# Optimization experiments

Hardware: AMD Instinct MI355X
Metric: run time of the kernel (lower is better)

## Reference

```python
import jax, jax.numpy as jnp
import numpy as np

H = 4096          # hidden_size
M = 4096          # num tokens
BLK = 128         # fp8 quant group/block size
EPS = 1e-6
FP8_MAX = 448.0   # float8_e4m3fn max


def fp8_round(x):
    # round-trip through fp8 e4m3 to emulate FP8 storage
    return x.astype(jnp.float8_e4m3fn).astype(jnp.float32)


def rms_norm(x, w, eps=EPS):
    var = jnp.mean(x * x, axis=-1, keepdims=True)
    return x * jax.lax.rsqrt(var + eps) * w


def block_fp8_linear(x, w, wscale):
    # per-token group-128 activation quant + 128x128 block-scaled fp8 GEMM
    m, k = x.shape
    kb = k // BLK
    nb = w.shape[1] // BLK
    xr = x.reshape(m, kb, BLK)
    amax = jnp.max(jnp.abs(xr), axis=-1)                      # [m, kb]
    s = jnp.maximum(amax, 1e-12) / FP8_MAX                    # group scales
    q = fp8_round(xr / s[..., None])                          # fp8 values
    xdq = (q * s[..., None]).reshape(m, k)                    # dequant acts
    # dequantize weight blockwise: w already fp8-valued floats
    wdq = (w.reshape(kb, BLK, nb, BLK) * wscale[:, None, :, None]).reshape(k, nb * BLK)
    return xdq @ wdq


def setup_inputs() -> dict:
    key = jax.random.key(0)
    ks = jax.random.split(key, 8)
    x = jax.random.normal(ks[0], (M, H), dtype=jnp.float32)
    sb = H // BLK
    d = {"x": x}
    for i in range(3):
        w = fp8_round(jax.random.uniform(ks[1 + i], (H, H), dtype=jnp.float32)).T
        d[f"w{i}"] = w
        d[f"ws{i}"] = jax.random.uniform(ks[4 + i], (sb, sb), dtype=jnp.float32)
    for i in range(4):
        d[f"nw{i}"] = jnp.ones((H,), dtype=jnp.float32)
    return d


def reference(x, w0, ws0, w1, ws1, w2, ws2, nw0, nw1, nw2, nw3):
    x = jax.nn.relu(x)
    resid = x
    y = rms_norm(x, nw0)
    x2 = block_fp8_linear(y, w0, ws0)
    resid = x2 + resid
    y2 = rms_norm(resid, nw1)
    x3 = block_fp8_linear(y2, w1, ws1)
    resid = x3 + resid
    y3 = rms_norm(resid, nw2)
    x4 = block_fp8_linear(y3, w2, ws2)
    resid = x4 + resid
    y4 = rms_norm(resid, nw3)
    return y4
```

## Files before the change

kernel.cpp:

```cpp
#include <hip/hip_runtime.h>
#include <stdint.h>

#define H 4096

typedef float v4f __attribute__((ext_vector_type(4)));
typedef long long i64;
typedef long long v2l __attribute__((ext_vector_type(2)));

__device__ __forceinline__ void gload16(const uint8_t* g, uint8_t* l) {
  __builtin_amdgcn_global_load_lds(
      (const __attribute__((address_space(1))) uint8_t*)g,
      (__attribute__((address_space(3))) uint8_t*)l, 16, 0, 0);
}

__device__ __forceinline__ int permpos(int kg) {
  const int kb = kg >> 7, b = kg & 127;
  const int ks = b >> 5, q = (b >> 3) & 3, j = b & 7;
  return kb * 128 + q * 32 + ks * 8 + j;
}

__global__ __launch_bounds__(256) void conv_w_kernel(
    const float* __restrict__ w0, const float* __restrict__ w1,
    const float* __restrict__ w2, uint8_t* __restrict__ o0,
    uint8_t* __restrict__ o1, uint8_t* __restrict__ o2) {
  const float* w = (blockIdx.z == 0) ? w0 : (blockIdx.z == 1 ? w1 : w2);
  uint8_t* o = (blockIdx.z == 0) ? o0 : (blockIdx.z == 1 ? o1 : o2);
  __shared__ uint8_t t[64][136];
  const int tid = threadIdx.x;
  const int k0 = blockIdx.y * 128, n0 = blockIdx.x * 64;
  const int rr = tid >> 4, cc = (tid & 15) * 4;
#pragma unroll
  for (int j = 0; j < 8; ++j) {
    const int r = rr + j * 16;
    v4f f = *(const v4f*)(w + (size_t)(k0 + r) * H + n0 + cc);
    unsigned p = __builtin_amdgcn_cvt_pk_fp8_f32(f.x, f.y, 0, false);
    p = __builtin_amdgcn_cvt_pk_fp8_f32(f.z, f.w, p, true);
    t[cc + 0][r] = p & 0xff;
    t[cc + 1][r] = (p >> 8) & 0xff;
    t[cc + 2][r] = (p >> 16) & 0xff;
    t[cc + 3][r] = p >> 24;
  }
  __syncthreads();
#pragma unroll
  for (int i = 0; i < 2; ++i) {
    const int c = i * 256 + tid;
    const int n = c >> 3, o16 = c & 7, q = o16 >> 1, h = o16 & 1;
    long long lo = *(const long long*)&t[n][64 * h + q * 8];
    long long hi = *(const long long*)&t[n][64 * h + 32 + q * 8];
    v2l val;
    val.x = lo;
    val.y = hi;
    *(v2l*)(o + (size_t)(n0 + n) * H + k0 + o16 * 16) = val;
  }
}

__global__ __launch_bounds__(256) void quant_kernel(
    const float* in, const float* __restrict__ nw, uint8_t* __restrict__ q,
    float* __restrict__ sxT, const int relu) {
  const int row = blockIdx.x, tid = threadIdx.x;
  const v4f* rp = (const v4f*)(in + (size_t)row * H);
  v4f v[4];
  float ss = 0.f;
#pragma unroll
  for (int j = 0; j < 4; ++j) {
    v4f x = rp[j * 256 + tid];
    if (relu) {
      x.x = fmaxf(x.x, 0.f); x.y = fmaxf(x.y, 0.f);
      x.z = fmaxf(x.z, 0.f); x.w = fmaxf(x.w, 0.f);
    }
    v[j] = x;
    ss += x.x * x.x + x.y * x.y + x.z * x.z + x.w * x.w;
  }
#pragma unroll
  for (int o = 32; o > 0; o >>= 1) ss += __shfl_down(ss, o);
  __shared__ float red[4];
  if ((tid & 63) == 0) red[tid >> 6] = ss;
  __syncthreads();
  ss = red[0] + red[1] + red[2] + red[3];
  const float rinv = 1.f / sqrtf(ss * (1.f / H) + 1e-6f);
#pragma unroll
  for (int j = 0; j < 4; ++j) {
    v4f nv = ((const v4f*)nw)[j * 256 + tid];
    v4f y;
    y.x = v[j].x * rinv * nv.x;
    y.y = v[j].y * rinv * nv.y;
    y.z = v[j].z * rinv * nv.z;
    y.w = v[j].w * rinv * nv.w;
    float am = fmaxf(fmaxf(fabsf(y.x), fabsf(y.y)), fmaxf(fabsf(y.z), fabsf(y.w)));
#pragma unroll
    for (int o = 16; o > 0; o >>= 1) am = fmaxf(am, __shfl_xor(am, o, 32));
    const float s = fmaxf(am, 1e-12f) / 448.f;
    unsigned p = __builtin_amdgcn_cvt_pk_fp8_f32(y.x / s, y.y / s, 0, false);
    p = __builtin_amdgcn_cvt_pk_fp8_f32(y.z / s, y.w / s, p, true);
    const int col = (j * 256 + tid) * 4;
    *(unsigned*)(q + (size_t)row * H + permpos(col)) = p;
    if ((tid & 31) == 0)
      sxT[(size_t)(j * 8 + (tid >> 5)) * 4096 + row] = s;
  }
}

__global__ __launch_bounds__(256) void norm_kernel(float* io,
                                                   const float* __restrict__ nw) {
  const int row = blockIdx.x, tid = threadIdx.x;
  v4f* rp = (v4f*)(io + (size_t)row * H);
  v4f v[4];
  float ss = 0.f;
#pragma unroll
  for (int j = 0; j < 4; ++j) {
    v4f x = rp[j * 256 + tid];
    v[j] = x;
    ss += x.x * x.x + x.y * x.y + x.z * x.z + x.w * x.w;
  }
#pragma unroll
  for (int o = 32; o > 0; o >>= 1) ss += __shfl_down(ss, o);
  __shared__ float red[4];
  if ((tid & 63) == 0) red[tid >> 6] = ss;
  __syncthreads();
  ss = red[0] + red[1] + red[2] + red[3];
  const float rinv = 1.f / sqrtf(ss * (1.f / H) + 1e-6f);
#pragma unroll
  for (int j = 0; j < 4; ++j) {
    v4f nv = ((const v4f*)nw)[j * 256 + tid];
    v4f y;
    y.x = v[j].x * rinv * nv.x;
    y.y = v[j].y * rinv * nv.y;
    y.z = v[j].z * rinv * nv.z;
    y.w = v[j].w * rinv * nv.w;
    rp[j * 256 + tid] = y;
  }
}

__global__ __launch_bounds__(256, 4) void gemm_kernel(
    const uint8_t* __restrict__ qa,
    const float* __restrict__ sxT,
    const uint8_t* __restrict__ wt,
    const float* __restrict__ ws,
    const float* resid, float* outp, const int relu) {
  __shared__ __attribute__((aligned(16))) uint8_t sA[16384];
  __shared__ __attribute__((aligned(16))) uint8_t sB[16384];
  __shared__ __attribute__((aligned(16))) float scb[128];
  __shared__ float ws_s[32];

  const int tid = threadIdx.x;
  const int n0 = blockIdx.x * 128, m0 = blockIdx.y * 128;
  if (tid < 32) ws_s[tid] = ws[tid * 32 + blockIdx.x];

  const int wv = tid >> 6, lane = tid & 63;
  const int quad = lane >> 4, l16 = lane & 15;
  const int wm = wv >> 1, wn = wv & 1;

  const int swc = (tid & 7) ^ ((tid >> 3) & 7);
  const uint8_t* gA = qa + (size_t)(m0 + (tid >> 3)) * H + swc * 16;
  const uint8_t* gB = wt + (size_t)(n0 + (tid >> 3)) * H + swc * 16;
  const uint8_t* gS = (const uint8_t*)sxT + (size_t)m0 * 4 + lane * 16;
  uint8_t* lA = sA + wv * 1024;
  uint8_t* lB = sB + wv * 1024;

  int offp[2];
#pragma unroll
  for (int ksp = 0; ksp < 2; ++ksp)
    offp[ksp] = (((quad * 2 + ksp) ^ (l16 & 7)) << 4);
  const int arow = (wm * 64 + l16) * 128;
  const int brow = (wn * 64 + l16) * 128;
  const int scoff = wm * 64 + quad * 4;

  const v4f zf = {0.f, 0.f, 0.f, 0.f};
  v4f acc[4][4];
#pragma unroll
  for (int i = 0; i < 4; ++i)
#pragma unroll
    for (int j = 0; j < 4; ++j) acc[i][j] = zf;

  for (int kb = 0; kb < 32; ++kb) {
#pragma unroll
    for (int i = 0; i < 4; ++i) {
      gload16(gA + (size_t)i * (32 * H), lA + i * 4096);
      gload16(gB + (size_t)i * (32 * H), lB + i * 4096);
    }
    if (wv == 0 && lane < 32) gload16(gS + (size_t)kb * 16384, (uint8_t*)scb);
    gA += 128;
    gB += 128;
    __syncthreads();

    const float wsk = ws_s[kb];
    v2l bf[4][2];
#pragma unroll
    for (int tc = 0; tc < 4; ++tc)
#pragma unroll
      for (int ksp = 0; ksp < 2; ++ksp)
        bf[tc][ksp] = *(const v2l*)(sB + brow + tc * 2048 + offp[ksp]);

#pragma unroll
    for (int tr = 0; tr < 4; ++tr) {
      const v2l a0 = *(const v2l*)(sA + arow + tr * 2048 + offp[0]);
      const v2l a1 = *(const v2l*)(sA + arow + tr * 2048 + offp[1]);
      const v4f s4 = *(const v4f*)(scb + scoff + tr * 16) * wsk;
#pragma unroll
      for (int tc = 0; tc < 4; ++tc) {
        v4f p = __builtin_amdgcn_mfma_f32_16x16x32_fp8_fp8(a0.x, bf[tc][0].x, zf, 0, 0, 0);
        p = __builtin_amdgcn_mfma_f32_16x16x32_fp8_fp8(a0.y, bf[tc][0].y, p, 0, 0, 0);
        p = __builtin_amdgcn_mfma_f32_16x16x32_fp8_fp8(a1.x, bf[tc][1].x, p, 0, 0, 0);
        p = __builtin_amdgcn_mfma_f32_16x16x32_fp8_fp8(a1.y, bf[tc][1].y, p, 0, 0, 0);
        acc[tr][tc] += p * s4;
      }
    }
    __syncthreads();
  }

  const int mB = m0 + wm * 64 + quad * 4;
  const int nB = n0 + wn * 64 + l16;
#pragma unroll
  for (int tr = 0; tr < 4; ++tr) {
#pragma unroll
    for (int r = 0; r < 4; ++r) {
      const size_t rowOff = (size_t)(mB + tr * 16 + r) * H;
#pragma unroll
      for (int tc = 0; tc < 4; ++tc) {
        const size_t idx = rowOff + nB + tc * 16;
        float rv = resid[idx];
        if (relu) rv = fmaxf(rv, 0.f);
        outp[idx] = acc[tr][tc][r] + rv;
      }
    }
  }
}

extern "C" void kernel_launch(void* const* d_in, const int* in_sizes, int n_in,
                              void* d_out, int out_size, void* d_ws, size_t ws_size,
                              hipStream_t stream) {
  const float* x   = (const float*)d_in[0];
  const float* w0  = (const float*)d_in[1];
  const float* ws0 = (const float*)d_in[2];
  const float* w1  = (const float*)d_in[3];
  const float* ws1 = (const float*)d_in[4];
  const float* w2  = (const float*)d_in[5];
  const float* ws2 = (const float*)d_in[6];
  const float* nw0 = (const float*)d_in[7];
  const float* nw1 = (const float*)d_in[8];
  const float* nw2 = (const float*)d_in[9];
  const float* nw3 = (const float*)d_in[10];
  float* R = (float*)d_out;

  uint8_t* base = (uint8_t*)d_ws;
  uint8_t* wq0 = base;
  uint8_t* wq1 = base + ((size_t)16 << 20);
  uint8_t* wq2 = base + ((size_t)32 << 20);
  uint8_t* qa  = base + ((size_t)48 << 20);
  float* sa    = (float*)(base + ((size_t)64 << 20));

  conv_w_kernel<<<dim3(64, 32, 3), 256, 0, stream>>>(w0, w1, w2, wq0, wq1, wq2);

  quant_kernel<<<4096, 256, 0, stream>>>(x, nw0, qa, sa, 1);
  gemm_kernel<<<dim3(32, 32), 256, 0, stream>>>(qa, sa, wq0, ws0, x, R, 1);

  quant_kernel<<<4096, 256, 0, stream>>>(R, nw1, qa, sa, 0);
  gemm_kernel<<<dim3(32, 32), 256, 0, stream>>>(qa, sa, wq1, ws1, R, R, 0);

  quant_kernel<<<4096, 256, 0, stream>>>(R, nw2, qa, sa, 0);
  gemm_kernel<<<dim3(32, 32), 256, 0, stream>>>(qa, sa, wq2, ws2, R, R, 0);

  norm_kernel<<<4096, 256, 0, stream>>>(R, nw3);
}
```

Measured before the change: 686.0 us.

## Fuse all stages into one persistent cooperative kernel with grid syncs

Refactors each kernel body into a grid-stride device stage and runs weight conversion, quantization, three GEMMs and the final norm inside one cooperative persistent kernel separated by grid.sync(). The aim is to remove the launch gaps and tail effects between eight separate launches. The trade-off is that the grid is capped at what fits resident (up to 1024 blocks), so the GEMM and row stages run as persistent loops. Grid-wide barriers also add their own cost. The original multi-launch path is kept as a fallback if the cooperative launch fails.

```diff
diff --git a/kernel.cpp b/kernel.cpp
--- a/kernel.cpp
+++ b/kernel.cpp
@@ -1,11 +1,13 @@
 #include <hip/hip_runtime.h>
+#include <hip/hip_cooperative_groups.h>
 #include <stdint.h>
 
 #define H 4096
 
 typedef float v4f __attribute__((ext_vector_type(4)));
-typedef long long i64;
 typedef long long v2l __attribute__((ext_vector_type(2)));
+
+namespace cg = cooperative_groups;
 
 __device__ __forceinline__ void gload16(const uint8_t* g, uint8_t* l) {
   __builtin_amdgcn_global_load_lds(
@@ -19,215 +21,287 @@
   return kb * 128 + q * 32 + ks * 8 + j;
 }
 
+
+__device__ void conv_stage(const float* __restrict__ w0,
+                           const float* __restrict__ w1,
+                           const float* __restrict__ w2, uint8_t* o0,
+                           uint8_t* o1, uint8_t* o2, uint8_t* smem, int bid,
+                           int nb) {
+  uint8_t(*t)[136] = reinterpret_cast<uint8_t(*)[136]>(smem);
+  const int tid = threadIdx.x;
+  const int rr = tid >> 4, cc = (tid & 15) * 4;
+  for (int g = bid; g < 6144; g += nb) {
+    const int z = g >> 11, rem = g & 2047;
+    const int k0 = (rem >> 6) * 128, n0 = (rem & 63) * 64;
+    const float* w = (z == 0) ? w0 : (z == 1 ? w1 : w2);
+    uint8_t* o = (z == 0) ? o0 : (z == 1 ? o1 : o2);
+#pragma unroll
+    for (int j = 0; j < 8; ++j) {
+      const int r = rr + j * 16;
+      v4f f = *(const v4f*)(w + (size_t)(k0 + r) * H + n0 + cc);
+      unsigned p = __builtin_amdgcn_cvt_pk_fp8_f32(f.x, f.y, 0, false);
+      p = __builtin_amdgcn_cvt_pk_fp8_f32(f.z, f.w, p, true);
+      t[cc + 0][r] = p & 0xff;
+      t[cc + 1][r] = (p >> 8) & 0xff;
+      t[cc + 2][r] = (p >> 16) & 0xff;
+      t[cc + 3][r] = p >> 24;
+    }
+    __syncthreads();
+#pragma unroll
+    for (int i = 0; i < 2; ++i) {
+      const int c = i * 256 + tid;
+      const int n = c >> 3, o16 = c & 7, q = o16 >> 1, h = o16 & 1;
+      long long lo = *(const long long*)&t[n][64 * h + q * 8];
+      long long hi = *(const long long*)&t[n][64 * h + 32 + q * 8];
+      v2l val;
+      val.x = lo;
+      val.y = hi;
+      *(v2l*)(o + (size_t)(n0 + n) * H + k0 + o16 * 16) = val;
+    }
+    __syncthreads();
+  }
+}
+
+__device__ void quant_stage(const float* in, const float* __restrict__ nw,
+                            uint8_t* __restrict__ q, float* __restrict__ sxT,
+                            const int relu, uint8_t* smem, int bid, int nb) {
+  float* red = reinterpret_cast<float*>(smem);
+  const int tid = threadIdx.x;
+  for (int row = bid; row < 4096; row += nb) {
+    const v4f* rp = (const v4f*)(in + (size_t)row * H);
+    v4f v[4];
+    float ss = 0.f;
+#pragma unroll
+    for (int j = 0; j < 4; ++j) {
+      v4f x = rp[j * 256 + tid];
+      if (relu) {
+        x.x = fmaxf(x.x, 0.f); x.y = fmaxf(x.y, 0.f);
+        x.z = fmaxf(x.z, 0.f); x.w = fmaxf(x.w, 0.f);
+      }
+      v[j] = x;
+      ss += x.x * x.x + x.y * x.y + x.z * x.z + x.w * x.w;
+    }
+#pragma unroll
+    for (int o = 32; o > 0; o >>= 1) ss += __shfl_down(ss, o);
+    if ((tid & 63) == 0) red[tid >> 6] = ss;
+    __syncthreads();
+    ss = red[0] + red[1] + red[2] + red[3];
+    const float rinv = 1.f / sqrtf(ss * (1.f / H) + 1e-6f);
+#pragma unroll
+    for (int j = 0; j < 4; ++j) {
+      v4f nv = ((const v4f*)nw)[j * 256 + tid];
+      v4f y;
+      y.x = v[j].x * rinv * nv.x;
+      y.y = v[j].y * rinv * nv.y;
+      y.z = v[j].z * rinv * nv.z;
+      y.w = v[j].w * rinv * nv.w;
+      float am =
+          fmaxf(fmaxf(fabsf(y.x), fabsf(y.y)), fmaxf(fabsf(y.z), fabsf(y.w)));
+#pragma unroll
+      for (int o = 16; o > 0; o >>= 1) am = fmaxf(am, __shfl_xor(am, o, 32));
+      const float s = fmaxf(am, 1e-12f) / 448.f;
+      unsigned p = __builtin_amdgcn_cvt_pk_fp8_f32(y.x / s, y.y / s, 0, false);
+      p = __builtin_amdgcn_cvt_pk_fp8_f32(y.z / s, y.w / s, p, true);
+      const int col = (j * 256 + tid) * 4;
+      *(unsigned*)(q + (size_t)row * H + permpos(col)) = p;
+      if ((tid & 31) == 0)
+        sxT[(size_t)(j * 8 + (tid >> 5)) * 4096 + row] = s;
+    }
+    __syncthreads();
+  }
+}
+
+__device__ void norm_stage(float* io, const float* __restrict__ nw,
+                           uint8_t* smem, int bid, int nb) {
+  float* red = reinterpret_cast<float*>(smem);
+  const int tid = threadIdx.x;
+  for (int row = bid; row < 4096; row += nb) {
+    v4f* rp = (v4f*)(io + (size_t)row * H);
+    v4f v[4];
+    float ss = 0.f;
+#pragma unroll
+    for (int j = 0; j < 4; ++j) {
+      v4f x = rp[j * 256 + tid];
+      v[j] = x;
+      ss += x.x * x.x + x.y * x.y + x.z * x.z + x.w * x.w;
+    }
+#pragma unroll
+    for (int o = 32; o > 0; o >>= 1) ss += __shfl_down(ss, o);
+    if ((tid & 63) == 0) red[tid >> 6] = ss;
+    __syncthreads();
+    ss = red[0] + red[1] + red[2] + red[3];
+    const float rinv = 1.f / sqrtf(ss * (1.f / H) + 1e-6f);
+#pragma unroll
+    for (int j = 0; j < 4; ++j) {
+      v4f nv = ((const v4f*)nw)[j * 256 + tid];
+      v4f y;
+      y.x = v[j].x * rinv * nv.x;
+      y.y = v[j].y * rinv * nv.y;
+      y.z = v[j].z * rinv * nv.z;
+      y.w = v[j].w * rinv * nv.w;
+      rp[j * 256 + tid] = y;
+    }
+    __syncthreads();
+  }
+}
+
+__device__ void gemm_stage(const uint8_t* __restrict__ qa,
+                           const float* __restrict__ sxT,
+                           const uint8_t* __restrict__ wt,
+                           const float* __restrict__ ws, const float* resid,
+                           float* outp, const int relu, uint8_t* smem, int bid,
+                           int nb) {
+  uint8_t* sA = smem;
+  uint8_t* sB = smem + 16384;
+  float* scb = reinterpret_cast<float*>(smem + 32768);
+  float* ws_s = reinterpret_cast<float*>(smem + 33280);
+  const int tid = threadIdx.x;
+  const int wv = tid >> 6, lane = tid & 63;
+  const int quad = lane >> 4, l16 = lane & 15;
+  const int wm = wv >> 1, wn = wv & 1;
+  const int swc = (tid & 7) ^ ((tid >> 3) & 7);
+
+  for (int b = bid; b < 1024; b += nb) {
+    const int n0 = (b & 31) * 128, m0 = (b >> 5) * 128;
+    if (tid < 32) ws_s[tid] = ws[tid * 32 + (b & 31)];
+
+    const uint8_t* gA = qa + (size_t)(m0 + (tid >> 3)) * H + swc * 16;
+    const uint8_t* gB = wt + (size_t)(n0 + (tid >> 3)) * H + swc * 16;
+    const uint8_t* gS = (const uint8_t*)sxT + (size_t)m0 * 4 + lane * 16;
+    uint8_t* lA = sA + wv * 1024;
+    uint8_t* lB = sB + wv * 1024;
+
+    int offp[2];
+#pragma unroll
+    for (int ksp = 0; ksp < 2; ++ksp)
+      offp[ksp] = (((quad * 2 + ksp) ^ (l16 & 7)) << 4);
+    const int arow = (wm * 64 + l16) * 128;
+    const int brow = (wn * 64 + l16) * 128;
+    const int scoff = wm * 64 + quad * 4;
+
+    const v4f zf = {0.f, 0.f, 0.f, 0.f};
+    v4f acc[4][4];
+#pragma unroll
+    for (int i = 0; i < 4; ++i)
+#pragma unroll
+      for (int j = 0; j < 4; ++j) acc[i][j] = zf;
+
+    for (int kb = 0; kb < 32; ++kb) {
+#pragma unroll
+      for (int i = 0; i < 4; ++i) {
+        gload16(gA + (size_t)i * (32 * H), lA + i * 4096);
+        gload16(gB + (size_t)i * (32 * H), lB + i * 4096);
+      }
+      if (wv == 0 && lane < 32) gload16(gS + (size_t)kb * 16384, (uint8_t*)scb);
+      gA += 128;
+      gB += 128;
+      __syncthreads();
+
+      const float wsk = ws_s[kb];
+      v2l bf[4][2];
+#pragma unroll
+      for (int tc = 0; tc < 4; ++tc)
+#pragma unroll
+        for (int ksp = 0; ksp < 2; ++ksp)
+          bf[tc][ksp] = *(const v2l*)(sB + brow + tc * 2048 + offp[ksp]);
+
+#pragma unroll
+      for (int tr = 0; tr < 4; ++tr) {
+        const v2l a0 = *(const v2l*)(sA + arow + tr * 2048 + offp[0]);
+        const v2l a1 = *(const v2l*)(sA + arow + tr * 2048 + offp[1]);
+        const v4f s4 = *(const v4f*)(scb + scoff + tr * 16) * wsk;
+#pragma unroll
+        for (int tc = 0; tc < 4; ++tc) {
+          v4f p = __builtin_amdgcn_mfma_f32_16x16x32_fp8_fp8(a0.x, bf[tc][0].x, zf, 0, 0, 0);
+          p = __builtin_amdgcn_mfma_f32_16x16x32_fp8_fp8(a0.y, bf[tc][0].y, p, 0, 0, 0);
+          p = __builtin_amdgcn_mfma_f32_16x16x32_fp8_fp8(a1.x, bf[tc][1].x, p, 0, 0, 0);
+          p = __builtin_amdgcn_mfma_f32_16x16x32_fp8_fp8(a1.y, bf[tc][1].y, p, 0, 0, 0);
+          acc[tr][tc] += p * s4;
+        }
+      }
+      __syncthreads();
+    }
+
+    const int mB = m0 + wm * 64 + quad * 4;
+    const int nB = n0 + wn * 64 + l16;
+#pragma unroll
+    for (int tr = 0; tr < 4; ++tr) {
+#pragma unroll
+      for (int r = 0; r < 4; ++r) {
+        const size_t rowOff = (size_t)(mB + tr * 16 + r) * H;
+#pragma unroll
+        for (int tc = 0; tc < 4; ++tc) {
+          const size_t idx = rowOff + nB + tc * 16;
+          float rv = resid[idx];
+          if (relu) rv = fmaxf(rv, 0.f);
+          outp[idx] = acc[tr][tc][r] + rv;
+        }
+      }
+    }
+  }
+}
+
+__global__ __launch_bounds__(256, 4) void mega_kernel(
+    const float* x, const float* w0, const float* ws0, const float* w1,
+    const float* ws1, const float* w2, const float* ws2, const float* nw0,
+    const float* nw1, const float* nw2, const float* nw3, float* R,
+    uint8_t* wq0, uint8_t* wq1, uint8_t* wq2, uint8_t* qa, float* sa) {
+  __shared__ __attribute__((aligned(16))) uint8_t smem[33792];
+  cg::grid_group grid = cg::this_grid();
+  const int bid = blockIdx.x, nb = gridDim.x;
+
+  conv_stage(w0, w1, w2, wq0, wq1, wq2, smem, bid, nb);
+  quant_stage(x, nw0, qa, sa, 1, smem, bid, nb);
+  grid.sync();
+  gemm_stage(qa, sa, wq0, ws0, x, R, 1, smem, bid, nb);
+  grid.sync();
+  quant_stage(R, nw1, qa, sa, 0, smem, bid, nb);
+  grid.sync();
+  gemm_stage(qa, sa, wq1, ws1, R, R, 0, smem, bid, nb);
+  grid.sync();
+  quant_stage(R, nw2, qa, sa, 0, smem, bid, nb);
+  grid.sync();
+  gemm_stage(qa, sa, wq2, ws2, R, R, 0, smem, bid, nb);
+  grid.sync();
+  norm_stage(R, nw3, smem, bid, nb);
+}
+
 __global__ __launch_bounds__(256) void conv_w_kernel(
     const float* __restrict__ w0, const float* __restrict__ w1,
     const float* __restrict__ w2, uint8_t* __restrict__ o0,
     uint8_t* __restrict__ o1, uint8_t* __restrict__ o2) {
-  const float* w = (blockIdx.z == 0) ? w0 : (blockIdx.z == 1 ? w1 : w2);
-  uint8_t* o = (blockIdx.z == 0) ? o0 : (blockIdx.z == 1 ? o1 : o2);
-  __shared__ uint8_t t[64][136];
-  const int tid = threadIdx.x;
-  const int k0 = blockIdx.y * 128, n0 = blockIdx.x * 64;
-  const int rr = tid >> 4, cc = (tid & 15) * 4;
-#pragma unroll
-  for (int j = 0; j < 8; ++j) {
-    const int r = rr + j * 16;
-    v4f f = *(const v4f*)(w + (size_t)(k0 + r) * H + n0 + cc);
-    unsigned p = __builtin_amdgcn_cvt_pk_fp8_f32(f.x, f.y, 0, false);
-    p = __builtin_amdgcn_cvt_pk_fp8_f32(f.z, f.w, p, true);
-    t[cc + 0][r] = p & 0xff;
-    t[cc + 1][r] = (p >> 8) & 0xff;
-    t[cc + 2][r] = (p >> 16) & 0xff;
-    t[cc + 3][r] = p >> 24;
-  }
-  __syncthreads();
-#pragma unroll
-  for (int i = 0; i < 2; ++i) {
-    const int c = i * 256 + tid;
-    const int n = c >> 3, o16 = c & 7, q = o16 >> 1, h = o16 & 1;
-    long long lo = *(const long long*)&t[n][64 * h + q * 8];
-    long long hi = *(const long long*)&t[n][64 * h + 32 + q * 8];
-    v2l val;
-    val.x = lo;
-    val.y = hi;
-    *(v2l*)(o + (size_t)(n0 + n) * H + k0 + o16 * 16) = val;
-  }
-}
-
-__global__ __launch_bounds__(256) void quant_kernel(
-    const float* in, const float* __restrict__ nw, uint8_t* __restrict__ q,
-    float* __restrict__ sxT, const int relu) {
-  const int row = blockIdx.x, tid = threadIdx.x;
-  const v4f* rp = (const v4f*)(in + (size_t)row * H);
-  v4f v[4];
-  float ss = 0.f;
-#pragma unroll
-  for (int j = 0; j < 4; ++j) {
-    v4f x = rp[j * 256 + tid];
-    if (relu) {
-      x.x = fmaxf(x.x, 0.f); x.y = fmaxf(x.y, 0.f);
-      x.z = fmaxf(x.z, 0.f); x.w = fmaxf(x.w, 0.f);
-    }
-    v[j] = x;
-    ss += x.x * x.x + x.y * x.y + x.z * x.z + x.w * x.w;
-  }
-#pragma unroll
-  for (int o = 32; o > 0; o >>= 1) ss += __shfl_down(ss, o);
-  __shared__ float red[4];
-  if ((tid & 63) == 0) red[tid >> 6] = ss;
-  __syncthreads();
-  ss = red[0] + red[1] + red[2] + red[3];
-  const float rinv = 1.f / sqrtf(ss * (1.f / H) + 1e-6f);
-#pragma unroll
-  for (int j = 0; j < 4; ++j) {
-    v4f nv = ((const v4f*)nw)[j * 256 + tid];
-    v4f y;
-    y.x = v[j].x * rinv * nv.x;
-    y.y = v[j].y * rinv * nv.y;
-    y.z = v[j].z * rinv * nv.z;
-    y.w = v[j].w * rinv * nv.w;
-    float am = fmaxf(fmaxf(fabsf(y.x), fabsf(y.y)), fmaxf(fabsf(y.z), fabsf(y.w)));
-#pragma unroll
-    for (int o = 16; o > 0; o >>= 1) am = fmaxf(am, __shfl_xor(am, o, 32));
-    const float s = fmaxf(am, 1e-12f) / 448.f;
-    unsigned p = __builtin_amdgcn_cvt_pk_fp8_f32(y.x / s, y.y / s, 0, false);
-    p = __builtin_amdgcn_cvt_pk_fp8_f32(y.z / s, y.w / s, p, true);
-    const int col = (j * 256 + tid) * 4;
-    *(unsigned*)(q + (size_t)row * H + permpos(col)) = p;
-    if ((tid & 31) == 0)
-      sxT[(size_t)(j * 8 + (tid >> 5)) * 4096 + row] = s;
-  }
+  __shared__ __attribute__((aligned(16))) uint8_t smem[8704];
+  const int g = (blockIdx.z << 11) | (blockIdx.y << 6) | blockIdx.x;
+  conv_stage(w0, w1, w2, o0, o1, o2, smem, g, 6144);
+}
+
+__global__ __launch_bounds__(256) void quant_kernel(const float* in,
+                                                    const float* __restrict__ nw,
+                                                    uint8_t* __restrict__ q,
+                                                    float* __restrict__ sxT,
+                                                    const int relu) {
+  __shared__ __attribute__((aligned(16))) uint8_t smem[16];
+  quant_stage(in, nw, q, sxT, relu, smem, blockIdx.x, 4096);
 }
 
 __global__ __launch_bounds__(256) void norm_kernel(float* io,
                                                    const float* __restrict__ nw) {
-  const int row = blockIdx.x, tid = threadIdx.x;
-  v4f* rp = (v4f*)(io + (size_t)row * H);
-  v4f v[4];
-  float ss = 0.f;
-#pragma unroll
-  for (int j = 0; j < 4; ++j) {
-    v4f x = rp[j * 256 + tid];
-    v[j] = x;
-    ss += x.x * x.x + x.y * x.y + x.z * x.z + x.w * x.w;
-  }
-#pragma unroll
-  for (int o = 32; o > 0; o >>= 1) ss += __shfl_down(ss, o);
-  __shared__ float red[4];
-  if ((tid & 63) == 0) red[tid >> 6] = ss;
-  __syncthreads();
-  ss = red[0] + red[1] + red[2] + red[3];
-  const float rinv = 1.f / sqrtf(ss * (1.f / H) + 1e-6f);
-#pragma unroll
-  for (int j = 0; j < 4; ++j) {
-    v4f nv = ((const v4f*)nw)[j * 256 + tid];
-    v4f y;
-    y.x = v[j].x * rinv * nv.x;
-    y.y = v[j].y * rinv * nv.y;
-    y.z = v[j].z * rinv * nv.z;
-    y.w = v[j].w * rinv * nv.w;
-    rp[j * 256 + tid] = y;
-  }
+  __shared__ __attribute__((aligned(16))) uint8_t smem[16];
+  norm_stage(io, nw, smem, blockIdx.x, 4096);
 }
 
 __global__ __launch_bounds__(256, 4) void gemm_kernel(
-    const uint8_t* __restrict__ qa,
-    const float* __restrict__ sxT,
-    const uint8_t* __restrict__ wt,
-    const float* __restrict__ ws,
+    const uint8_t* __restrict__ qa, const float* __restrict__ sxT,
+    const uint8_t* __restrict__ wt, const float* __restrict__ ws,
     const float* resid, float* outp, const int relu) {
-  __shared__ __attribute__((aligned(16))) uint8_t sA[16384];
-  __shared__ __attribute__((aligned(16))) uint8_t sB[16384];
-  __shared__ __attribute__((aligned(16))) float scb[128];
-  __shared__ float ws_s[32];
-
-  const int tid = threadIdx.x;
-  const int n0 = blockIdx.x * 128, m0 = blockIdx.y * 128;
-  if (tid < 32) ws_s[tid] = ws[tid * 32 + blockIdx.x];
-
-  const int wv = tid >> 6, lane = tid & 63;
-  const int quad = lane >> 4, l16 = lane & 15;
-  const int wm = wv >> 1, wn = wv & 1;
-
-  const int swc = (tid & 7) ^ ((tid >> 3) & 7);
-  const uint8_t* gA = qa + (size_t)(m0 + (tid >> 3)) * H + swc * 16;
-  const uint8_t* gB = wt + (size_t)(n0 + (tid >> 3)) * H + swc * 16;
-  const uint8_t* gS = (const uint8_t*)sxT + (size_t)m0 * 4 + lane * 16;
-  uint8_t* lA = sA + wv * 1024;
-  uint8_t* lB = sB + wv * 1024;
-
-  int offp[2];
-#pragma unroll
-  for (int ksp = 0; ksp < 2; ++ksp)
-    offp[ksp] = (((quad * 2 + ksp) ^ (l16 & 7)) << 4);
-  const int arow = (wm * 64 + l16) * 128;
-  const int brow = (wn * 64 + l16) * 128;
-  const int scoff = wm * 64 + quad * 4;
-
-  const v4f zf = {0.f, 0.f, 0.f, 0.f};
-  v4f acc[4][4];
-#pragma unroll
-  for (int i = 0; i < 4; ++i)
-#pragma unroll
-    for (int j = 0; j < 4; ++j) acc[i][j] = zf;
-
-  for (int kb = 0; kb < 32; ++kb) {
-#pragma unroll
-    for (int i = 0; i < 4; ++i) {
-      gload16(gA + (size_t)i * (32 * H), lA + i * 4096);
-      gload16(gB + (size_t)i * (32 * H), lB + i * 4096);
-    }
-    if (wv == 0 && lane < 32) gload16(gS + (size_t)kb * 16384, (uint8_t*)scb);
-    gA += 128;
-    gB += 128;
-    __syncthreads();
-
-    const float wsk = ws_s[kb];
-    v2l bf[4][2];
-#pragma unroll
-    for (int tc = 0; tc < 4; ++tc)
-#pragma unroll
-      for (int ksp = 0; ksp < 2; ++ksp)
-        bf[tc][ksp] = *(const v2l*)(sB + brow + tc * 2048 + offp[ksp]);
-
-#pragma unroll
-    for (int tr = 0; tr < 4; ++tr) {
-      const v2l a0 = *(const v2l*)(sA + arow + tr * 2048 + offp[0]);
-      const v2l a1 = *(const v2l*)(sA + arow + tr * 2048 + offp[1]);
-      const v4f s4 = *(const v4f*)(scb + scoff + tr * 16) * wsk;
-#pragma unroll
-      for (int tc = 0; tc < 4; ++tc) {
-        v4f p = __builtin_amdgcn_mfma_f32_16x16x32_fp8_fp8(a0.x, bf[tc][0].x, zf, 0, 0, 0);
-        p = __builtin_amdgcn_mfma_f32_16x16x32_fp8_fp8(a0.y, bf[tc][0].y, p, 0, 0, 0);
-        p = __builtin_amdgcn_mfma_f32_16x16x32_fp8_fp8(a1.x, bf[tc][1].x, p, 0, 0, 0);
-        p = __builtin_amdgcn_mfma_f32_16x16x32_fp8_fp8(a1.y, bf[tc][1].y, p, 0, 0, 0);
-        acc[tr][tc] += p * s4;
-      }
-    }
-    __syncthreads();
-  }
-
-  const int mB = m0 + wm * 64 + quad * 4;
-  const int nB = n0 + wn * 64 + l16;
-#pragma unroll
-  for (int tr = 0; tr < 4; ++tr) {
-#pragma unroll
-    for (int r = 0; r < 4; ++r) {
-      const size_t rowOff = (size_t)(mB + tr * 16 + r) * H;
-#pragma unroll
-      for (int tc = 0; tc < 4; ++tc) {
-        const size_t idx = rowOff + nB + tc * 16;
-        float rv = resid[idx];
-        if (relu) rv = fmaxf(rv, 0.f);
-        outp[idx] = acc[tr][tc][r] + rv;
-      }
-    }
-  }
+  __shared__ __attribute__((aligned(16))) uint8_t smem[33792];
+  gemm_stage(qa, sxT, wt, ws, resid, outp, relu, smem,
+             blockIdx.y * 32 + blockIdx.x, 1024);
 }
 
 extern "C" void kernel_launch(void* const* d_in, const int* in_sizes, int n_in,
-                              void* d_out, int out_size, void* d_ws, size_t ws_size,
-                              hipStream_t stream) {
+                              void* d_out, int out_size, void* d_ws,
+                              size_t ws_size, hipStream_t stream) {
   const float* x   = (const float*)d_in[0];
   const float* w0  = (const float*)d_in[1];
   const float* ws0 = (const float*)d_in[2];
@@ -248,16 +322,36 @@
   uint8_t* qa  = base + ((size_t)48 << 20);
   float* sa    = (float*)(base + ((size_t)64 << 20));
 
-  conv_w_kernel<<<dim3(64, 32, 3), 256, 0, stream>>>(w0, w1, w2, wq0, wq1, wq2);
-
-  quant_kernel<<<4096, 256, 0, stream>>>(x, nw0, qa, sa, 1);
-  gemm_kernel<<<dim3(32, 32), 256, 0, stream>>>(qa, sa, wq0, ws0, x, R, 1);
-
-  quant_kernel<<<4096, 256, 0, stream>>>(R, nw1, qa, sa, 0);
-  gemm_kernel<<<dim3(32, 32), 256, 0, stream>>>(qa, sa, wq1, ws1, R, R, 0);
-
-  quant_kernel<<<4096, 256, 0, stream>>>(R, nw2, qa, sa, 0);
-  gemm_kernel<<<dim3(32, 32), 256, 0, stream>>>(qa, sa, wq2, ws2, R, R, 0);
-
-  norm_kernel<<<4096, 256, 0, stream>>>(R, nw3);
-}
+  static int grid_blocks = -1;
+  if (grid_blocks < 0) {
+    int per_cu = 0;
+    if (hipOccupancyMaxActiveBlocksPerMultiprocessor(
+            &per_cu, (const void*)mega_kernel, 256, 0) != hipSuccess ||
+        per_cu < 1)
+      per_cu = 0;
+    long long mb = (long long)per_cu * 256;
+    grid_blocks = (int)(mb > 1024 ? 1024 : mb);
+  }
+
+  bool ok = false;
+  if (grid_blocks >= 256) {
+    void* args[] = {(void*)&x,   (void*)&w0,  (void*)&ws0, (void*)&w1,
+                    (void*)&ws1, (void*)&w2,  (void*)&ws2, (void*)&nw0,
+                    (void*)&nw1, (void*)&nw2, (void*)&nw3, (void*)&R,
+                    (void*)&wq0, (void*)&wq1, (void*)&wq2, (void*)&qa,
+                    (void*)&sa};
+    ok = hipLaunchCooperativeKernel((const void*)mega_kernel,
+                                    dim3(grid_blocks), dim3(256), args, 0,
+                                    stream) == hipSuccess;
+  }
+  if (!ok) {
+    conv_w_kernel<<<dim3(64, 32, 3), 256, 0, stream>>>(w0, w1, w2, wq0, wq1, wq2);
+    quant_kernel<<<4096, 256, 0, stream>>>(x, nw0, qa, sa, 1);
+    gemm_kernel<<<dim3(32, 32), 256, 0, stream>>>(qa, sa, wq0, ws0, x, R, 1);
+    quant_kernel<<<4096, 256, 0, stream>>>(R, nw1, qa, sa, 0);
+    gemm_kernel<<<dim3(32, 32), 256, 0, stream>>>(qa, sa, wq1, ws1, R, R, 0);
+    quant_kernel<<<4096, 256, 0, stream>>>(R, nw2, qa, sa, 0);
+    gemm_kernel<<<dim3(32, 32), 256, 0, stream>>>(qa, sa, wq2, ws2, R, R, 0);
+    norm_kernel<<<4096, 256, 0, stream>>>(R, nw3);
+  }
+}
```

Result: slower. 1.671 ms (+143.5%).

## Fuse RMSNorm/quant into GEMM tail via per-row-block atomic counters

Applied to the files above, without the earlier changes.

Weight fp8 conversion and the first activation quantisation are merged into one prep kernel. Each GEMM now ends with an atomic counter per 128-row block. The last 16 tiles of a row block wait until all 32 column tiles are done, then run the next layer's RMSNorm+quant, or the final norm, for 8 rows each. This removes four standalone launches and the gaps between them, but adds spin-waiting and relies on all blocks being co-resident to avoid deadlock.

```diff
diff --git a/kernel.cpp b/kernel.cpp
--- a/kernel.cpp
+++ b/kernel.cpp
@@ -4,7 +4,6 @@
 #define H 4096
 
 typedef float v4f __attribute__((ext_vector_type(4)));
-typedef long long i64;
 typedef long long v2l __attribute__((ext_vector_type(2)));
 
 __device__ __forceinline__ void gload16(const uint8_t* g, uint8_t* l) {
@@ -19,15 +18,11 @@
   return kb * 128 + q * 32 + ks * 8 + j;
 }
 
-__global__ __launch_bounds__(256) void conv_w_kernel(
-    const float* __restrict__ w0, const float* __restrict__ w1,
-    const float* __restrict__ w2, uint8_t* __restrict__ o0,
-    uint8_t* __restrict__ o1, uint8_t* __restrict__ o2) {
-  const float* w = (blockIdx.z == 0) ? w0 : (blockIdx.z == 1 ? w1 : w2);
-  uint8_t* o = (blockIdx.z == 0) ? o0 : (blockIdx.z == 1 ? o1 : o2);
-  __shared__ uint8_t t[64][136];
+__device__ __forceinline__ void conv_tile(const float* __restrict__ w,
+                                          uint8_t* __restrict__ o, int k0,
+                                          int n0, uint8_t* smem) {
+  uint8_t(*t)[136] = reinterpret_cast<uint8_t(*)[136]>(smem);
   const int tid = threadIdx.x;
-  const int k0 = blockIdx.y * 128, n0 = blockIdx.x * 64;
   const int rr = tid >> 4, cc = (tid & 15) * 4;
 #pragma unroll
   for (int j = 0; j < 8; ++j) {
@@ -54,10 +49,11 @@
   }
 }
 
-__global__ __launch_bounds__(256) void quant_kernel(
-    const float* in, const float* __restrict__ nw, uint8_t* __restrict__ q,
-    float* __restrict__ sxT, const int relu) {
-  const int row = blockIdx.x, tid = threadIdx.x;
+__device__ __forceinline__ void quant_row(const float* in,
+                                          const float* __restrict__ nw,
+                                          uint8_t* q, float* sxT, int row,
+                                          int relu, float* red) {
+  const int tid = threadIdx.x;
   const v4f* rp = (const v4f*)(in + (size_t)row * H);
   v4f v[4];
   float ss = 0.f;
@@ -73,7 +69,6 @@
   }
 #pragma unroll
   for (int o = 32; o > 0; o >>= 1) ss += __shfl_down(ss, o);
-  __shared__ float red[4];
   if ((tid & 63) == 0) red[tid >> 6] = ss;
   __syncthreads();
   ss = red[0] + red[1] + red[2] + red[3];
@@ -86,7 +81,8 @@
     y.y = v[j].y * rinv * nv.y;
     y.z = v[j].z * rinv * nv.z;
     y.w = v[j].w * rinv * nv.w;
-    float am = fmaxf(fmaxf(fabsf(y.x), fabsf(y.y)), fmaxf(fabsf(y.z), fabsf(y.w)));
+    float am =
+        fmaxf(fmaxf(fabsf(y.x), fabsf(y.y)), fmaxf(fabsf(y.z), fabsf(y.w)));
 #pragma unroll
     for (int o = 16; o > 0; o >>= 1) am = fmaxf(am, __shfl_xor(am, o, 32));
     const float s = fmaxf(am, 1e-12f) / 448.f;
@@ -99,9 +95,9 @@
   }
 }
 
-__global__ __launch_bounds__(256) void norm_kernel(float* io,
-                                                   const float* __restrict__ nw) {
-  const int row = blockIdx.x, tid = threadIdx.x;
+__device__ __forceinline__ void norm_row(float* io, const float* __restrict__ nw,
+                                         int row, float* red) {
+  const int tid = threadIdx.x;
   v4f* rp = (v4f*)(io + (size_t)row * H);
   v4f v[4];
   float ss = 0.f;
@@ -113,7 +109,6 @@
   }
 #pragma unroll
   for (int o = 32; o > 0; o >>= 1) ss += __shfl_down(ss, o);
-  __shared__ float red[4];
   if ((tid & 63) == 0) red[tid >> 6] = ss;
   __syncthreads();
   ss = red[0] + red[1] + red[2] + red[3];
@@ -130,16 +125,40 @@
   }
 }
 
-__global__ __launch_bounds__(256, 4) void gemm_kernel(
-    const uint8_t* __restrict__ qa,
-    const float* __restrict__ sxT,
+__global__ __launch_bounds__(256) void prep_kernel(
+    const float* __restrict__ w0, const float* __restrict__ w1,
+    const float* __restrict__ w2, uint8_t* __restrict__ o0,
+    uint8_t* __restrict__ o1, uint8_t* __restrict__ o2, const float* x,
+    const float* __restrict__ nw0, uint8_t* qa, float* sa, int* sync0) {
+  __shared__ __attribute__((aligned(16))) uint8_t smem[8704];
+  const int bid = blockIdx.x;
+  if (bid == 0) {
+    for (int i = threadIdx.x; i < 3072; i += 256) sync0[i] = 0;
+  }
+  if (bid < 6144) {
+    const int z = bid >> 11, rem = bid & 2047;
+    const float* w = (z == 0) ? w0 : (z == 1 ? w1 : w2);
+    uint8_t* o = (z == 0) ? o0 : (z == 1 ? o1 : o2);
+    conv_tile(w, o, (rem >> 6) * 128, (rem & 63) * 64, smem);
+  } else {
+    quant_row(x, nw0, qa, sa, bid - 6144, 1, (float*)smem);
+  }
+}
+
+__global__ __launch_bounds__(256, 4) void gemm_fused_kernel(
+    const uint8_t* qa,
+    const float* sxT,
     const uint8_t* __restrict__ wt,
     const float* __restrict__ ws,
-    const float* resid, float* outp, const int relu) {
-  __shared__ __attribute__((aligned(16))) uint8_t sA[16384];
-  __shared__ __attribute__((aligned(16))) uint8_t sB[16384];
-  __shared__ __attribute__((aligned(16))) float scb[128];
-  __shared__ float ws_s[32];
+    const float* resid, float* outp, const int relu,
+    int* cnt,
+    const int tailmode,
+    uint8_t* qa2, float* sa2, const float* __restrict__ nwt) {
+  __shared__ __attribute__((aligned(16))) uint8_t smem[33792];
+  uint8_t* sA = smem;
+  uint8_t* sB = smem + 16384;
+  float* scb = reinterpret_cast<float*>(smem + 32768);
+  float* ws_s = reinterpret_cast<float*>(smem + 33280);
 
   const int tid = threadIdx.x;
   const int n0 = blockIdx.x * 128, m0 = blockIdx.y * 128;
@@ -223,11 +242,38 @@
       }
     }
   }
+
+  __threadfence();
+  __shared__ int rank_s;
+  if (tid == 0) rank_s = atomicAdd(&cnt[m0 >> 7], 1);
+  __syncthreads();
+  const int rank = rank_s;
+  if (rank < 16) return;
+
+  if (rank < 31) {
+    if (tid == 0) {
+      while (__hip_atomic_load(&cnt[m0 >> 7], __ATOMIC_ACQUIRE,
+                               __HIP_MEMORY_SCOPE_AGENT) < 32)
+        __builtin_amdgcn_s_sleep(8);
+    }
+    __syncthreads();
+  }
+  __threadfence();
+
+  float* red = scb;
+  const int rb = m0 + (rank - 16) * 8;
+  for (int r = rb; r < rb + 8; ++r) {
+    if (tailmode == 0)
+      quant_row(outp, nwt, qa2, sa2, r, 0, red);
+    else
+      norm_row(outp, nwt, r, red);
+    __syncthreads();
+  }
 }
 
 extern "C" void kernel_launch(void* const* d_in, const int* in_sizes, int n_in,
-                              void* d_out, int out_size, void* d_ws, size_t ws_size,
-                              hipStream_t stream) {
+                              void* d_out, int out_size, void* d_ws,
+                              size_t ws_size, hipStream_t stream) {
   const float* x   = (const float*)d_in[0];
   const float* w0  = (const float*)d_in[1];
   const float* ws0 = (const float*)d_in[2];
@@ -247,17 +293,18 @@
   uint8_t* wq2 = base + ((size_t)32 << 20);
   uint8_t* qa  = base + ((size_t)48 << 20);
   float* sa    = (float*)(base + ((size_t)64 << 20));
-
-  conv_w_kernel<<<dim3(64, 32, 3), 256, 0, stream>>>(w0, w1, w2, wq0, wq1, wq2);
-
-  quant_kernel<<<4096, 256, 0, stream>>>(x, nw0, qa, sa, 1);
-  gemm_kernel<<<dim3(32, 32), 256, 0, stream>>>(qa, sa, wq0, ws0, x, R, 1);
-
-  quant_kernel<<<4096, 256, 0, stream>>>(R, nw1, qa, sa, 0);
-  gemm_kernel<<<dim3(32, 32), 256, 0, stream>>>(qa, sa, wq1, ws1, R, R, 0);
-
-  quant_kernel<<<4096, 256, 0, stream>>>(R, nw2, qa, sa, 0);
-  gemm_kernel<<<dim3(32, 32), 256, 0, stream>>>(qa, sa, wq2, ws2, R, R, 0);
-
-  norm_kernel<<<4096, 256, 0, stream>>>(R, nw3);
-}
+  int* sync0   = (int*)(base + ((size_t)65 << 20));
+
+  prep_kernel<<<10240, 256, 0, stream>>>(w0, w1, w2, wq0, wq1, wq2, x, nw0, qa,
+                                         sa, sync0);
+
+  int* c0 = sync0;
+  int* c1 = sync0 + 1024;
+  int* c2 = sync0 + 2048;
+  gemm_fused_kernel<<<dim3(32, 32), 256, 0, stream>>>(
+      qa, sa, wq0, ws0, x, R, 1, c0, 0, qa, sa, nw1);
+  gemm_fused_kernel<<<dim3(32, 32), 256, 0, stream>>>(
+      qa, sa, wq1, ws1, R, R, 0, c1, 0, qa, sa, nw2);
+  gemm_fused_kernel<<<dim3(32, 32), 256, 0, stream>>>(
+      qa, sa, wq2, ws2, R, R, 0, c2, 1, qa, sa, nw3);
+}
```

After: 1.454 ms. +112.0%, slower.
